# Optimization experiments

Hardware: AMD Instinct MI355X
Metric: run time of the kernel (lower is better)

Reference implementation:

```python
import jax, jax.numpy as jnp
import numpy as np

N = 4096       # num_nodes (must equal out_features: final div broadcasts [C,N]/[N,1])
IN_F = 1024    # module in_features
OUT_F = 4096   # module out_features == N
F_RAW = 512    # raw node feature dim fed to the in-forward Linear


def setup_inputs() -> dict:
    key = jax.random.key(0)
    ks = jax.random.split(key, 5)
    node_features = jax.random.normal(ks[0], (N, F_RAW), dtype=jnp.float32)
    adjacency_matrix = jax.random.bernoulli(ks[1], 0.004, (N, N)).astype(jnp.float32)
    eye = jnp.eye(N, dtype=jnp.float32)
    A0 = adjacency_matrix * (1.0 - eye)                 # adjacency w/o self loops
    S = (A0 @ A0 + A0) * (1.0 - eye)                    # sibling matrix, zero diag
    mask_hadamard = S[:, None, :]                       # [N,1,N]
    mask_father = adjacency_matrix[:, None, :]          # [N,1,N]
    neighbor_count = jnp.maximum(A0.sum(axis=1, keepdims=True), 1.0)  # [N,1]
    lim = float(1.0 / np.sqrt(F_RAW))
    linear_w = jax.random.uniform(ks[2], (IN_F, F_RAW), minval=-lim, maxval=lim, dtype=jnp.float32)
    linear_b = jax.random.uniform(ks[3], (IN_F,), minval=-lim, maxval=lim, dtype=jnp.float32)
    weight = jax.random.normal(ks[4], (IN_F, OUT_F), dtype=jnp.float32) * float(np.sqrt(2.0 / IN_F))
    return dict(node_features=node_features, adjacency_matrix=adjacency_matrix,
                mask_father=mask_father, neighbor_count=neighbor_count,
                mask_hadamard=mask_hadamard, linear_w=linear_w, linear_b=linear_b,
                weight=weight)


def reference(node_features, adjacency_matrix, mask_father, neighbor_count,
              mask_hadamard, linear_w, linear_b, weight):
    # Linear + projection: wf[n,c]
    x = node_features @ linear_w.T + linear_b           # [N, IN_F]
    wf = x @ weight                                      # [N, C]
    # Original builds masked_hadamard[j,i,c] = wf[i,c]*wf[j,c]*S[i,j] ([N,C,N]),
    # contracts with adjacency over i, masks with adj[k,j], sums over k:
    #   sum_hadamard[c,j] = wf[j,c] * sum_i (sum_k adj[k,j]*adj[k,i]) * S[i,j] * wf[i,c]
    # Fused form avoids the O(N^2 C) intermediates; same math.
    A_out = mask_father[:, 0, :]                         # adj[k,j]  [N,N]
    S = mask_hadamard[:, 0, :]                           # S[i,j]    [N,N]
    G = A_out.T @ adjacency_matrix                       # G[j,i] = sum_k adj[k,j]*adj[k,i]
    P = G * S.T                                          # P[j,i] = G[j,i]*S[i,j]
    sum_hadamard = (wf * (P @ wf)).T                     # [C, N]
    # Final broadcast division exactly as torch: [C,N] / [N,1] (requires C==N)
    return sum_hadamard / jnp.square(neighbor_count)
```

## Files before the change

kernel.cpp:

```cpp
#include <hip/hip_runtime.h>
#include <hip/hip_bf16.h>

typedef __attribute__((ext_vector_type(8))) short s16x8;
typedef __attribute__((ext_vector_type(4))) float f32x4;
typedef __attribute__((ext_vector_type(8))) unsigned short u16x8;

__device__ __forceinline__ float b2f(unsigned short u) {
  union { unsigned int i; float f; } x; x.i = ((unsigned int)u) << 16; return x.f;
}
__device__ __forceinline__ unsigned short f2b(float f) {
  __hip_bfloat16 h = __float2bfloat16(f);
  return *reinterpret_cast<unsigned short*>(&h);
}

#define TILE 128
#define BK 32
#define PCAP 128
#define SCAP 1024

template <int EPI>
__device__ __forceinline__ void gemm_body(
    unsigned short* As, unsigned short* Bs,
    int bx, int by,
    const unsigned short* __restrict__ A,
    const unsigned short* __restrict__ B,
    unsigned short* __restrict__ C,
    int M, int N, int K,
    const float* __restrict__ epi_f)
{
  const int tid  = threadIdx.x;
  const int lane = tid & 63;
  const int wave = tid >> 6;
  const int wm = (wave & 1) * 64;
  const int wn = (wave >> 1) * 64;
  const long bm = (long)by * TILE;
  const long bn = (long)bx * TILE;

  f32x4 acc[4][4] = {};

  auto STAGE = [&](int kt, int b) {
    const long kb = (long)kt * BK;
#pragma unroll
    for (int i = 0; i < 2; ++i) {
      const int c0 = (wave * 2 + i) * 64;
      const int c  = c0 + lane;
      const int r  = c >> 2;
      const int cc = ((c & 3) ^ ((c >> 3) & 3)) * 8;
      const unsigned short* ga = A + (bm + r) * (long)K + kb + cc;
      const unsigned short* gb = B + (bn + r) * (long)K + kb + cc;
      __builtin_amdgcn_global_load_lds(
          (const __attribute__((address_space(1))) void*)ga,
          (__attribute__((address_space(3))) void*)(As + b * (TILE * BK) + c0 * 8), 16, 0, 0);
      __builtin_amdgcn_global_load_lds(
          (const __attribute__((address_space(1))) void*)gb,
          (__attribute__((address_space(3))) void*)(Bs + b * (TILE * BK) + c0 * 8), 16, 0, 0);
    }
  };

  const int kTiles = K / BK;
  STAGE(0, 0);

  for (int kt = 0; kt < kTiles; ++kt) {
    const int cur = kt & 1;
    if (kt + 1 < kTiles) {
      STAGE(kt + 1, cur ^ 1);
      asm volatile("s_waitcnt vmcnt(4)" ::: "memory");
    } else {
      asm volatile("s_waitcnt vmcnt(0)" ::: "memory");
    }
    __builtin_amdgcn_sched_barrier(0);
    __builtin_amdgcn_s_barrier();
    __builtin_amdgcn_sched_barrier(0);

    const int rl = lane & 15;
    const int kqx = ((lane >> 4) ^ ((rl >> 1) & 3)) * 8;
    s16x8 af[4], bfr[4];
#pragma unroll
    for (int mi = 0; mi < 4; ++mi)
      af[mi] = *(const s16x8*)(As + cur * (TILE * BK) + (wm + mi * 16 + rl) * BK + kqx);
#pragma unroll
    for (int ni = 0; ni < 4; ++ni)
      bfr[ni] = *(const s16x8*)(Bs + cur * (TILE * BK) + (wn + ni * 16 + rl) * BK + kqx);
#pragma unroll
    for (int mi = 0; mi < 4; ++mi)
#pragma unroll
      for (int ni = 0; ni < 4; ++ni)
        acc[mi][ni] = __builtin_amdgcn_mfma_f32_16x16x32_bf16(af[mi], bfr[ni], acc[mi][ni], 0, 0, 0);

    __builtin_amdgcn_sched_barrier(0);
    __builtin_amdgcn_s_barrier();
    __builtin_amdgcn_sched_barrier(0);
  }

  const int cl = lane & 15;
  const int rq = (lane >> 4) * 4;
#pragma unroll
  for (int mi = 0; mi < 4; ++mi)
#pragma unroll
    for (int ni = 0; ni < 4; ++ni)
#pragma unroll
      for (int r = 0; r < 4; ++r) {
        const long row = bm + wm + mi * 16 + rq + r;
        const long col = bn + wn + ni * 16 + cl;
        float v = acc[mi][ni][r];
        if (EPI == 1) v += epi_f[col];
        C[row * (long)N + col] = f2b(v);
      }
}

template <int EPI>
__global__ __launch_bounds__(256) void gemm_nt(
    const unsigned short* __restrict__ A,
    const unsigned short* __restrict__ B,
    unsigned short* __restrict__ C,
    int M, int N, int K,
    const float* __restrict__ epi_f)
{
  __shared__ unsigned short As[2 * TILE * BK];
  __shared__ unsigned short Bs[2 * TILE * BK];
  gemm_body<EPI>(As, Bs, blockIdx.x, blockIdx.y, A, B, C, M, N, K, epi_f);
}

__device__ __forceinline__ void colbits_body(
    int i, const float* __restrict__ adj, unsigned long long* __restrict__ colb)
{
  const int t = threadIdx.x;
  const unsigned long long bit = 1ull << (i & 63);
  const int w = i >> 6;
  const float* r = adj + (long)i * 4096;
#pragma unroll
  for (int q = 0; q < 4; ++q) {
    int c = (t + q * 256) * 4;
    float4 v = *(const float4*)(r + c);
    if (v.x != 0.f) atomicOr(&colb[(long)(c + 0) * 64 + w], bit);
    if (v.y != 0.f) atomicOr(&colb[(long)(c + 1) * 64 + w], bit);
    if (v.z != 0.f) atomicOr(&colb[(long)(c + 2) * 64 + w], bit);
    if (v.w != 0.f) atomicOr(&colb[(long)(c + 3) * 64 + w], bit);
  }
}

__global__ __launch_bounds__(256) void build_P2(
    const float* __restrict__ S, const unsigned long long* __restrict__ colb,
    int* __restrict__ pk, float* __restrict__ pv, int* __restrict__ pcnt)
{
  const int k = blockIdx.x;
  const int t = threadIdx.x;
  const int lane = t & 63;
  __shared__ __align__(16) unsigned long long ck[64];
  __shared__ int jl[SCAP];
  __shared__ float sl[SCAP];
  __shared__ int m;
  if (t == 0) m = 0;
  if (t < 64) ck[t] = colb[(long)k * 64 + t];
  __syncthreads();
  const float* Sr = S + (long)k * 4096;
  const unsigned long long lmask = (1ull << lane) - 1ull;
#pragma unroll
  for (int q = 0; q < 4; ++q) {
    int c = (t + q * 256) * 4;
    float4 v = *(const float4*)(Sr + c);
    float vals[4] = { v.x, v.y, v.z, v.w };
#pragma unroll
    for (int r = 0; r < 4; ++r) {
      float vv = vals[r];
      unsigned long long mask = __ballot(vv != 0.f);
      if (mask) {
        int base;
        if (lane == 0) base = atomicAdd(&m, __popcll(mask));
        base = __shfl(base, 0, 64);
        if (vv != 0.f) {
          int pos = base + __popcll(mask & lmask);
          if (pos < SCAP) { jl[pos] = c + r; sl[pos] = vv; }
        }
      }
    }
  }
  __syncthreads();
  const int mm = min(m, SCAP);
  const int l = t & 7;
  for (int idx = (t >> 3); idx < mm; idx += 32) {
    const int j = jl[idx];
    const ulonglong2* cj = (const ulonglong2*)(colb + (long)j * 64);
    int cnt = 0;
#pragma unroll
    for (int it = 0; it < 4; ++it) {
      ulonglong2 q  = cj[it * 8 + l];
      ulonglong2 cc = *(const ulonglong2*)&ck[it * 16 + l * 2];
      cnt += __popcll(q.x & cc.x) + __popcll(q.y & cc.y);
    }
    cnt += __shfl_down(cnt, 4, 8);
    cnt += __shfl_down(cnt, 2, 8);
    cnt += __shfl_down(cnt, 1, 8);
    if (l == 0 && cnt > 0) {
      int slot = atomicAdd(&pcnt[j], 1);
      if (slot < PCAP) {
        pk[(long)j * PCAP + slot] = k;
        pv[(long)j * PCAP + slot] = (float)cnt * sl[idx];
      }
    }
  }
}

__device__ __forceinline__ void transpose64_f2b(
    const float* __restrict__ in, unsigned short* __restrict__ out,
    int R, int C, long r0, long c0, unsigned short (*tile)[66])
{
  const int t = threadIdx.x;
#pragma unroll
  for (int i = 0; i < 4; ++i) {
    int v = t + i * 256;
    int r = v >> 4;
    int c = (v & 15) * 4;
    float4 d = *(const float4*)(in + (r0 + r) * (long)C + c0 + c);
    tile[r][c + 0] = f2b(d.x); tile[r][c + 1] = f2b(d.y);
    tile[r][c + 2] = f2b(d.z); tile[r][c + 3] = f2b(d.w);
  }
  __syncthreads();
#pragma unroll
  for (int i = 0; i < 4; ++i) {
    int v = t + i * 256;
    int r = v >> 4;
    int c = (v & 15) * 4;
    ushort4 d;
    d.x = tile[c + 0][r]; d.y = tile[c + 1][r]; d.z = tile[c + 2][r]; d.w = tile[c + 3][r];
    *(ushort4*)(out + (c0 + r) * (long)R + r0 + c) = d;
  }
}

__global__ __launch_bounds__(256) void prep_fused(
    const float* __restrict__ w,  unsigned short* __restrict__ weightT,
    const float* __restrict__ nf, unsigned short* __restrict__ nfb,
    const float* __restrict__ lw, unsigned short* __restrict__ lwbT,
    float* __restrict__ zp,
    const float* __restrict__ lb, float* __restrict__ b2)
{
  __shared__ unsigned short tile[64][66];
  const int b = blockIdx.x;
  const int t = threadIdx.x;
  if (b < 1024) {
    transpose64_f2b(w, weightT, 1024, 4096, (long)(b >> 6) * 64, (long)(b & 63) * 64, tile);
  } else if (b < 3072) {
    const long e = ((long)(b - 1024) * 256 + t) * 4;
    float4 d = *(const float4*)(nf + e);
    ushort4 o;
    o.x = f2b(d.x); o.y = f2b(d.y); o.z = f2b(d.z); o.w = f2b(d.w);
    *(ushort4*)(nfb + e) = o;
  } else if (b < 3200) {
    const int idx = b - 3072;
    transpose64_f2b(lw, lwbT, 1024, 512, (long)(idx >> 3) * 64, (long)(idx & 7) * 64, tile);
  } else if (b < 3716) {
    const long e = ((long)(b - 3200) * 256 + t) * 4;
    *(float4*)(zp + e) = make_float4(0.f, 0.f, 0.f, 0.f);
  } else {
    const int n = (b - 3716) * 256 + t;
    float acc = 0.f;
    for (int k = 0; k < 1024; k += 4) {
      acc += lb[k]     * w[(long)k * 4096 + n]
           + lb[k + 1] * w[(long)(k + 1) * 4096 + n]
           + lb[k + 2] * w[(long)(k + 2) * 4096 + n]
           + lb[k + 3] * w[(long)(k + 3) * 4096 + n];
    }
    b2[n] = acc;
  }
}

__global__ __launch_bounds__(256) void gw2_colbits(
    const unsigned short* __restrict__ weightT, const unsigned short* __restrict__ lwbT,
    unsigned short* __restrict__ W2T,
    const float* __restrict__ adj, unsigned long long* __restrict__ colb)
{
  extern __shared__ ulonglong2 dsm[];
  const int b = blockIdx.x;
  if (b < 128) {
    unsigned short* As = (unsigned short*)dsm;
    unsigned short* Bs = As + 2 * TILE * BK;
    gemm_body<0>(As, Bs, b & 3, b >> 2, weightT, lwbT, W2T, 4096, 512, 1024, nullptr);
  } else {
    colbits_body(b - 128, adj, colb);
  }
}

__global__ __launch_bounds__(256) void spmm_fused(
    const int* __restrict__ pk, const float* __restrict__ pv,
    const int* __restrict__ pcnt, const unsigned short* __restrict__ wf,
    const float* __restrict__ nc, float* __restrict__ VO)
{
  __shared__ int   k_l[4][PCAP];
  __shared__ float v_l[4][PCAP];
  __shared__ int   n_s[4];
  const int t = threadIdx.x;
  const int wave = t >> 6;
  const int lane = t & 63;
  const int seg = blockIdx.x;
  const int jb  = blockIdx.y * 4;
  {
    int e0 = t;
    k_l[e0 >> 7][e0 & 127] = pk[(long)(jb + (e0 >> 7)) * PCAP + (e0 & 127)];
    v_l[e0 >> 7][e0 & 127] = pv[(long)(jb + (e0 >> 7)) * PCAP + (e0 & 127)];
    int e1 = t + 256;
    k_l[e1 >> 7][e1 & 127] = pk[(long)(jb + (e1 >> 7)) * PCAP + (e1 & 127)];
    v_l[e1 >> 7][e1 & 127] = pv[(long)(jb + (e1 >> 7)) * PCAP + (e1 & 127)];
    if (t < 4) n_s[t] = min(pcnt[jb + t], PCAP);
  }
  __syncthreads();
  const int j = jb + wave;
  const int n = n_s[wave];
  const int* __restrict__ kk = k_l[wave];
  const float* __restrict__ vv = v_l[wave];
  const int c0 = seg * 512 + lane * 8;

  float acc[8] = {};
  int m = 0;
  for (; m + 8 <= n; m += 8) {
    float vs[8];
    u16x8 d[8];
#pragma unroll
    for (int r = 0; r < 8; ++r) {
      vs[r] = vv[m + r];
      d[r] = *(const u16x8*)(wf + (unsigned)(kk[m + r] * 4096 + c0));
    }
    __builtin_amdgcn_sched_barrier(0);
#pragma unroll
    for (int r = 0; r < 8; ++r)
#pragma unroll
      for (int q = 0; q < 8; ++q)
        acc[q] += vs[r] * b2f(d[r][q]);
  }
  for (; m + 2 <= n; m += 2) {
    const float v0 = vv[m], v1 = vv[m + 1];
    u16x8 a = *(const u16x8*)(wf + (unsigned)(kk[m]     * 4096 + c0));
    u16x8 b = *(const u16x8*)(wf + (unsigned)(kk[m + 1] * 4096 + c0));
#pragma unroll
    for (int q = 0; q < 8; ++q) acc[q] += v0 * b2f(a[q]) + v1 * b2f(b[q]);
  }
  for (; m < n; ++m) {
    const float va = vv[m];
    u16x8 a = *(const u16x8*)(wf + (unsigned)(kk[m] * 4096 + c0));
#pragma unroll
    for (int q = 0; q < 8; ++q) acc[q] += va * b2f(a[q]);
  }
  u16x8 wa = *(const u16x8*)(wf + (unsigned)(j * 4096 + c0));
  float out[8];
#pragma unroll
  for (int q = 0; q < 8; q += 4) {
    float4 nv = *(const float4*)(nc + c0 + q);
    float n4[4] = { nv.x, nv.y, nv.z, nv.w };
#pragma unroll
    for (int r = 0; r < 4; ++r)
      out[q + r] = acc[q + r] * b2f(wa[q + r]) / (n4[r] * n4[r]);
  }
  float* dst = VO + (long)j * 4096 + c0;
  *(float4*)(dst + 0) = make_float4(out[0], out[1], out[2], out[3]);
  *(float4*)(dst + 4) = make_float4(out[4], out[5], out[6], out[7]);
}

__global__ __launch_bounds__(256) void final_transpose(float* __restrict__ D)
{
  const int bx = blockIdx.x, by = blockIdx.y;
  if (by > bx) return;
  const int X = bx * 64, Y = by * 64;
  const bool diag = (bx == by);
  __shared__ float t1[64][65];
  __shared__ float t2[64][65];
  const int t = threadIdx.x;
  const int r0 = t >> 4;
  const int c4 = (t & 15) * 4;
#pragma unroll
  for (int i = 0; i < 4; ++i) {
    int r = r0 + i * 16;
    float4 d = *(const float4*)&D[(long)(Y + r) * 4096 + X + c4];
    t1[r][c4 + 0] = d.x; t1[r][c4 + 1] = d.y; t1[r][c4 + 2] = d.z; t1[r][c4 + 3] = d.w;
    if (!diag) {
      float4 e = *(const float4*)&D[(long)(X + r) * 4096 + Y + c4];
      t2[r][c4 + 0] = e.x; t2[r][c4 + 1] = e.y; t2[r][c4 + 2] = e.z; t2[r][c4 + 3] = e.w;
    }
  }
  __syncthreads();
#pragma unroll
  for (int i = 0; i < 4; ++i) {
    int r = r0 + i * 16;
    float4 o;
    o.x = t1[c4 + 0][r]; o.y = t1[c4 + 1][r]; o.z = t1[c4 + 2][r]; o.w = t1[c4 + 3][r];
    *(float4*)&D[(long)(X + r) * 4096 + Y + c4] = o;
    if (!diag) {
      float4 p;
      p.x = t2[c4 + 0][r]; p.y = t2[c4 + 1][r]; p.z = t2[c4 + 2][r]; p.w = t2[c4 + 3][r];
      *(float4*)&D[(long)(Y + r) * 4096 + X + c4] = p;
    }
  }
}

extern "C" void kernel_launch(void* const* d_in, const int* in_sizes, int n_in,
                              void* d_out, int out_size, void* d_ws, size_t ws_size,
                              hipStream_t stream) {
  const float* nf  = (const float*)d_in[0];
  const float* adj = (const float*)d_in[1];
  const float* nc  = (const float*)d_in[3];
  const float* S   = (const float*)d_in[4];
  const float* lw  = (const float*)d_in[5];
  const float* lb  = (const float*)d_in[6];
  const float* w   = (const float*)d_in[7];

  char* ws = (char*)d_ws;
  unsigned short*      wf      = (unsigned short*)(ws);
  unsigned long long*  colb    = (unsigned long long*)(ws + (32ll << 20));
  int*                 pcnt    = (int*)(ws + (34ll << 20));
  int*                 pk      = (int*)(ws + (35ll << 20));
  float*               pv      = (float*)(ws + (37ll << 20));
  unsigned short*      weightT = (unsigned short*)(ws + (40ll << 20));
  unsigned short*      nfb     = (unsigned short*)(ws + (48ll << 20));
  unsigned short*      lwbT    = (unsigned short*)(ws + (52ll << 20));
  unsigned short*      W2T     = (unsigned short*)(ws + (54ll << 20));
  float*               b2      = (float*)(ws + (58ll << 20));
  float*               VO      = (float*)d_out;

  prep_fused<<<3732, 256, 0, stream>>>(w, weightT, nf, nfb, lw, lwbT, (float*)colb, lb, b2);
  gw2_colbits<<<4224, 256, 32768, stream>>>(weightT, lwbT, W2T, adj, colb);
  build_P2<<<4096, 256, 0, stream>>>(S, colb, pk, pv, pcnt);
  gemm_nt<1><<<dim3(32, 32), 256, 0, stream>>>(nfb, W2T, wf, 4096, 4096, 512, b2);
  spmm_fused<<<dim3(8, 1024), 256, 0, stream>>>(pk, pv, pcnt, wf, nc, VO);
  final_transpose<<<dim3(64, 64), 256, 0, stream>>>(VO);
}
```

Measured before the change: 387.5 us.

## Fuse output transpose into SpMM epilogue via shared-memory staging; move bias GEMV

The SpMM kernel now handles 16 rows per block over four rounds and stages the results in a shared-memory tile. It then writes them transposed straight into the output, so the separate in-place transpose kernel and its extra 64 MB read/write pass are gone. The division by the squared neighbor count becomes a precomputed reciprocal multiply. The bias-projection GEMV moves from the prep kernel into the gw2_colbits launch. The cost is fewer SpMM blocks, a roughly 33 KB shared tile per block that lowers occupancy, and output stores that are only 16 bytes contiguous per row.

```diff
diff --git a/kernel.cpp b/kernel.cpp
--- a/kernel.cpp
+++ b/kernel.cpp
@@ -231,8 +231,7 @@
     const float* __restrict__ w,  unsigned short* __restrict__ weightT,
     const float* __restrict__ nf, unsigned short* __restrict__ nfb,
     const float* __restrict__ lw, unsigned short* __restrict__ lwbT,
-    float* __restrict__ zp,
-    const float* __restrict__ lb, float* __restrict__ b2)
+    float* __restrict__ zp)
 {
   __shared__ unsigned short tile[64][66];
   const int b = blockIdx.x;
@@ -248,11 +247,28 @@
   } else if (b < 3200) {
     const int idx = b - 3072;
     transpose64_f2b(lw, lwbT, 1024, 512, (long)(idx >> 3) * 64, (long)(idx & 7) * 64, tile);
-  } else if (b < 3716) {
+  } else {
     const long e = ((long)(b - 3200) * 256 + t) * 4;
     *(float4*)(zp + e) = make_float4(0.f, 0.f, 0.f, 0.f);
+  }
+}
+
+__global__ __launch_bounds__(256) void gw2_colbits(
+    const unsigned short* __restrict__ weightT, const unsigned short* __restrict__ lwbT,
+    unsigned short* __restrict__ W2T,
+    const float* __restrict__ adj, unsigned long long* __restrict__ colb,
+    const float* __restrict__ lb, const float* __restrict__ w, float* __restrict__ b2)
+{
+  extern __shared__ ulonglong2 dsm[];
+  const int b = blockIdx.x;
+  if (b < 128) {
+    unsigned short* As = (unsigned short*)dsm;
+    unsigned short* Bs = As + 2 * TILE * BK;
+    gemm_body<0>(As, Bs, b & 3, b >> 2, weightT, lwbT, W2T, 4096, 512, 1024, nullptr);
+  } else if (b < 4224) {
+    colbits_body(b - 128, adj, colb);
   } else {
-    const int n = (b - 3716) * 256 + t;
+    const int n = (b - 4224) * 256 + threadIdx.x;
     float acc = 0.f;
     for (int k = 0; k < 1024; k += 4) {
       acc += lb[k]     * w[(long)k * 4096 + n]
@@ -264,129 +280,99 @@
   }
 }
 
-__global__ __launch_bounds__(256) void gw2_colbits(
-    const unsigned short* __restrict__ weightT, const unsigned short* __restrict__ lwbT,
-    unsigned short* __restrict__ W2T,
-    const float* __restrict__ adj, unsigned long long* __restrict__ colb)
-{
-  extern __shared__ ulonglong2 dsm[];
-  const int b = blockIdx.x;
-  if (b < 128) {
-    unsigned short* As = (unsigned short*)dsm;
-    unsigned short* Bs = As + 2 * TILE * BK;
-    gemm_body<0>(As, Bs, b & 3, b >> 2, weightT, lwbT, W2T, 4096, 512, 1024, nullptr);
-  } else {
-    colbits_body(b - 128, adj, colb);
-  }
-}
-
-__global__ __launch_bounds__(256) void spmm_fused(
+__global__ __launch_bounds__(256) void spmm_t(
     const int* __restrict__ pk, const float* __restrict__ pv,
     const int* __restrict__ pcnt, const unsigned short* __restrict__ wf,
-    const float* __restrict__ nc, float* __restrict__ VO)
+    const float* __restrict__ nc, float* __restrict__ OUT)
 {
   __shared__ int   k_l[4][PCAP];
   __shared__ float v_l[4][PCAP];
   __shared__ int   n_s[4];
+  __shared__ float o_l[16][516];
   const int t = threadIdx.x;
   const int wave = t >> 6;
   const int lane = t & 63;
   const int seg = blockIdx.x;
-  const int jb  = blockIdx.y * 4;
+  const int jb0 = blockIdx.y * 16;
+  const int c0 = seg * 512 + lane * 8;
+
+  float inv2[8];
   {
-    int e0 = t;
-    k_l[e0 >> 7][e0 & 127] = pk[(long)(jb + (e0 >> 7)) * PCAP + (e0 & 127)];
-    v_l[e0 >> 7][e0 & 127] = pv[(long)(jb + (e0 >> 7)) * PCAP + (e0 & 127)];
-    int e1 = t + 256;
-    k_l[e1 >> 7][e1 & 127] = pk[(long)(jb + (e1 >> 7)) * PCAP + (e1 & 127)];
-    v_l[e1 >> 7][e1 & 127] = pv[(long)(jb + (e1 >> 7)) * PCAP + (e1 & 127)];
-    if (t < 4) n_s[t] = min(pcnt[jb + t], PCAP);
-  }
-  __syncthreads();
-  const int j = jb + wave;
-  const int n = n_s[wave];
-  const int* __restrict__ kk = k_l[wave];
-  const float* __restrict__ vv = v_l[wave];
-  const int c0 = seg * 512 + lane * 8;
-
-  float acc[8] = {};
-  int m = 0;
-  for (; m + 8 <= n; m += 8) {
-    float vs[8];
-    u16x8 d[8];
-#pragma unroll
-    for (int r = 0; r < 8; ++r) {
-      vs[r] = vv[m + r];
-      d[r] = *(const u16x8*)(wf + (unsigned)(kk[m + r] * 4096 + c0));
-    }
-    __builtin_amdgcn_sched_barrier(0);
-#pragma unroll
-    for (int r = 0; r < 8; ++r)
-#pragma unroll
-      for (int q = 0; q < 8; ++q)
-        acc[q] += vs[r] * b2f(d[r][q]);
-  }
-  for (; m + 2 <= n; m += 2) {
-    const float v0 = vv[m], v1 = vv[m + 1];
-    u16x8 a = *(const u16x8*)(wf + (unsigned)(kk[m]     * 4096 + c0));
-    u16x8 b = *(const u16x8*)(wf + (unsigned)(kk[m + 1] * 4096 + c0));
-#pragma unroll
-    for (int q = 0; q < 8; ++q) acc[q] += v0 * b2f(a[q]) + v1 * b2f(b[q]);
-  }
-  for (; m < n; ++m) {
-    const float va = vv[m];
-    u16x8 a = *(const u16x8*)(wf + (unsigned)(kk[m] * 4096 + c0));
-#pragma unroll
-    for (int q = 0; q < 8; ++q) acc[q] += va * b2f(a[q]);
-  }
-  u16x8 wa = *(const u16x8*)(wf + (unsigned)(j * 4096 + c0));
-  float out[8];
-#pragma unroll
-  for (int q = 0; q < 8; q += 4) {
-    float4 nv = *(const float4*)(nc + c0 + q);
-    float n4[4] = { nv.x, nv.y, nv.z, nv.w };
-#pragma unroll
-    for (int r = 0; r < 4; ++r)
-      out[q + r] = acc[q + r] * b2f(wa[q + r]) / (n4[r] * n4[r]);
-  }
-  float* dst = VO + (long)j * 4096 + c0;
-  *(float4*)(dst + 0) = make_float4(out[0], out[1], out[2], out[3]);
-  *(float4*)(dst + 4) = make_float4(out[4], out[5], out[6], out[7]);
-}
-
-__global__ __launch_bounds__(256) void final_transpose(float* __restrict__ D)
-{
-  const int bx = blockIdx.x, by = blockIdx.y;
-  if (by > bx) return;
-  const int X = bx * 64, Y = by * 64;
-  const bool diag = (bx == by);
-  __shared__ float t1[64][65];
-  __shared__ float t2[64][65];
-  const int t = threadIdx.x;
-  const int r0 = t >> 4;
-  const int c4 = (t & 15) * 4;
-#pragma unroll
-  for (int i = 0; i < 4; ++i) {
-    int r = r0 + i * 16;
-    float4 d = *(const float4*)&D[(long)(Y + r) * 4096 + X + c4];
-    t1[r][c4 + 0] = d.x; t1[r][c4 + 1] = d.y; t1[r][c4 + 2] = d.z; t1[r][c4 + 3] = d.w;
-    if (!diag) {
-      float4 e = *(const float4*)&D[(long)(X + r) * 4096 + Y + c4];
-      t2[r][c4 + 0] = e.x; t2[r][c4 + 1] = e.y; t2[r][c4 + 2] = e.z; t2[r][c4 + 3] = e.w;
-    }
-  }
-  __syncthreads();
-#pragma unroll
-  for (int i = 0; i < 4; ++i) {
-    int r = r0 + i * 16;
-    float4 o;
-    o.x = t1[c4 + 0][r]; o.y = t1[c4 + 1][r]; o.z = t1[c4 + 2][r]; o.w = t1[c4 + 3][r];
-    *(float4*)&D[(long)(X + r) * 4096 + Y + c4] = o;
-    if (!diag) {
-      float4 p;
-      p.x = t2[c4 + 0][r]; p.y = t2[c4 + 1][r]; p.z = t2[c4 + 2][r]; p.w = t2[c4 + 3][r];
-      *(float4*)&D[(long)(Y + r) * 4096 + X + c4] = p;
-    }
+    float4 na = *(const float4*)(nc + c0);
+    float4 nb = *(const float4*)(nc + c0 + 4);
+    float nn[8] = { na.x, na.y, na.z, na.w, nb.x, nb.y, nb.z, nb.w };
+#pragma unroll
+    for (int q = 0; q < 8; ++q) inv2[q] = 1.f / (nn[q] * nn[q]);
+  }
+
+  for (int rd = 0; rd < 4; ++rd) {
+    const int jb = jb0 + rd * 4;
+    {
+      int e0 = t;
+      k_l[e0 >> 7][e0 & 127] = pk[(long)(jb + (e0 >> 7)) * PCAP + (e0 & 127)];
+      v_l[e0 >> 7][e0 & 127] = pv[(long)(jb + (e0 >> 7)) * PCAP + (e0 & 127)];
+      int e1 = t + 256;
+      k_l[e1 >> 7][e1 & 127] = pk[(long)(jb + (e1 >> 7)) * PCAP + (e1 & 127)];
+      v_l[e1 >> 7][e1 & 127] = pv[(long)(jb + (e1 >> 7)) * PCAP + (e1 & 127)];
+      if (t < 4) n_s[t] = min(pcnt[jb + t], PCAP);
+    }
+    __syncthreads();
+    const int j = jb + wave;
+    const int n = n_s[wave];
+    const int* __restrict__ kk = k_l[wave];
+    const float* __restrict__ vv = v_l[wave];
+
+    float acc[8] = {};
+    int m = 0;
+    for (; m + 8 <= n; m += 8) {
+      float vs[8];
+      u16x8 d[8];
+#pragma unroll
+      for (int r = 0; r < 8; ++r) {
+        vs[r] = vv[m + r];
+        d[r] = *(const u16x8*)(wf + (unsigned)(kk[m + r] * 4096 + c0));
+      }
+      __builtin_amdgcn_sched_barrier(0);
+#pragma unroll
+      for (int r = 0; r < 8; ++r)
+#pragma unroll
+        for (int q = 0; q < 8; ++q)
+          acc[q] += vs[r] * b2f(d[r][q]);
+    }
+    for (; m + 2 <= n; m += 2) {
+      const float v0 = vv[m], v1 = vv[m + 1];
+      u16x8 a = *(const u16x8*)(wf + (unsigned)(kk[m]     * 4096 + c0));
+      u16x8 b = *(const u16x8*)(wf + (unsigned)(kk[m + 1] * 4096 + c0));
+#pragma unroll
+      for (int q = 0; q < 8; ++q) acc[q] += v0 * b2f(a[q]) + v1 * b2f(b[q]);
+    }
+    for (; m < n; ++m) {
+      const float va = vv[m];
+      u16x8 a = *(const u16x8*)(wf + (unsigned)(kk[m] * 4096 + c0));
+#pragma unroll
+      for (int q = 0; q < 8; ++q) acc[q] += va * b2f(a[q]);
+    }
+    u16x8 wa = *(const u16x8*)(wf + (unsigned)(j * 4096 + c0));
+    float out[8];
+#pragma unroll
+    for (int q = 0; q < 8; ++q) out[q] = acc[q] * b2f(wa[q]) * inv2[q];
+    float* orow = &o_l[rd * 4 + wave][lane * 8];
+    *(float4*)(orow)     = make_float4(out[0], out[1], out[2], out[3]);
+    *(float4*)(orow + 4) = make_float4(out[4], out[5], out[6], out[7]);
+    __syncthreads();
+  }
+
+  const long i0 = (long)seg * 512;
+  const int jq = (lane & 3) * 4;
+#pragma unroll
+  for (int ch = 0; ch < 8; ++ch) {
+    const int row = wave * 128 + ch * 16 + (lane >> 2);
+    float4 vq;
+    vq.x = o_l[jq + 0][row];
+    vq.y = o_l[jq + 1][row];
+    vq.z = o_l[jq + 2][row];
+    vq.w = o_l[jq + 3][row];
+    *(float4*)&OUT[(i0 + row) * 4096 + jb0 + jq] = vq;
   }
 }
 
@@ -414,10 +400,9 @@
   float*               b2      = (float*)(ws + (58ll << 20));
   float*               VO      = (float*)d_out;
 
-  prep_fused<<<3732, 256, 0, stream>>>(w, weightT, nf, nfb, lw, lwbT, (float*)colb, lb, b2);
-  gw2_colbits<<<4224, 256, 32768, stream>>>(weightT, lwbT, W2T, adj, colb);
+  prep_fused<<<3716, 256, 0, stream>>>(w, weightT, nf, nfb, lw, lwbT, (float*)colb);
+  gw2_colbits<<<4240, 256, 32768, stream>>>(weightT, lwbT, W2T, adj, colb, lb, w, b2);
   build_P2<<<4096, 256, 0, stream>>>(S, colb, pk, pv, pcnt);
   gemm_nt<1><<<dim3(32, 32), 256, 0, stream>>>(nfb, W2T, wf, 4096, 4096, 512, b2);
-  spmm_fused<<<dim3(8, 1024), 256, 0, stream>>>(pk, pv, pcnt, wf, nc, VO);
-  final_transpose<<<dim3(64, 64), 256, 0, stream>>>(VO);
-}
+  spmm_t<<<dim3(8, 256), 256, 0, stream>>>(pk, pv, pcnt, wf, nc, VO);
+}
```

Result: faster. 379.5 us (-2.1%).
